# Performance work log

Hardware: AMD Instinct MI355X
Metric: run time of the kernel (lower is better)

## Reference

```python
import jax, jax.numpy as jnp
import numpy as np

NUM_HEADS = 12


def setup_inputs() -> dict:
    key = jax.random.key(0)
    ks = jax.random.split(key, 6)
    B, N, C, CNN = 64, 576, 768, 2048
    return {
        "image_patches": jax.random.normal(ks[0], (B, N, C), dtype=jnp.float32),
        "cnn_feature_vector": jax.random.normal(ks[1], (B, CNN), dtype=jnp.float32),
        "Wq": jax.random.normal(ks[2], (C, C), dtype=jnp.float32) * (C ** -0.5),
        "Wkv": jax.random.normal(ks[3], (CNN, 2 * C), dtype=jnp.float32) * (CNN ** -0.5),
        "Wp": jax.random.normal(ks[4], (C, C), dtype=jnp.float32) * (C ** -0.5),
        "bp": jnp.zeros((C,), dtype=jnp.float32),
    }


def reference(image_patches, cnn_feature_vector, Wq, Wkv, Wp, bp):
    B, N, C = image_patches.shape
    H = NUM_HEADS
    D = C // H
    scale = D ** -0.5
    # Q projection: [B, N, C] -> [B, N, H, D]
    q = (image_patches @ Wq).reshape(B, N, H, D)
    # KV projection from single CNN feature (KV seq len == 1): [B, 2C]
    kv = cnn_feature_vector @ Wkv
    k = kv[:, :C].reshape(B, H, D)  # [B, H, D]
    v = kv[:, C:].reshape(B, H, D)  # [B, H, D]
    # attn logits: q . k over head_dim -> [B, N, H, 1]; softmax over kv_len=1
    logits = jnp.einsum("bnhd,bhd->bnh", q, k)[..., None] * scale
    attn = jax.nn.softmax(logits, axis=-1)  # degenerate: all ones
    # attn @ v with kv_len 1 -> broadcast v over N
    x = (attn * v[:, None, :, :]).reshape(B, N, C)
    # output projection (dropout is identity in eval)
    return x @ Wp + bp
```

## Files before the change

kernel.cpp:

```cpp
#include <hip/hip_runtime.h>


#define B_DIM   64
#define N_DIM   576
#define C_DIM   768
#define CNN_DIM 2048
#define C4_DIM  192

typedef float f4 __attribute__((ext_vector_type(4)));

__global__ __launch_bounds__(256) void proj_v_kernel(
    const float* __restrict__ cnn, const float* __restrict__ Wkv,
    float* __restrict__ v)
{
    __shared__ f4 red[32 * 64];

    int tid = threadIdx.x;
    int c4l = tid & 7;
    int s   = tid >> 3;
    int bg  = blockIdx.x & 7;
    int cg  = blockIdx.x >> 3;
    int b0  = bg * 8;
    int c4  = cg * 8 + c4l;
    int k0  = s * 64;

    const f4* w4 = (const f4*)(Wkv + C_DIM);

    f4 acc[8];
#pragma unroll
    for (int i = 0; i < 8; ++i) acc[i] = (f4)0.f;

#pragma unroll 4
    for (int kk = 0; kk < 64; ++kk) {
        int k = k0 + kk;
        f4 w = w4[k * 384 + c4];
#pragma unroll
        for (int i = 0; i < 8; ++i) {
            float a = cnn[(b0 + i) * CNN_DIM + k];
            acc[i] += a * w;
        }
    }

#pragma unroll
    for (int i = 0; i < 8; ++i) red[s * 64 + i * 8 + c4l] = acc[i];
    __syncthreads();

#pragma unroll
    for (int step = 16; step >= 1; step >>= 1) {
        if (s < step) {
#pragma unroll
            for (int i = 0; i < 8; ++i)
                red[s * 64 + i * 8 + c4l] += red[(s + step) * 64 + i * 8 + c4l];
        }
        __syncthreads();
    }

    if (tid < 64) {
        int i  = tid >> 3;
        int cl = tid & 7;
        *(f4*)(v + (b0 + i) * C_DIM + (cg * 8 + cl) * 4) = red[i * 8 + cl];
    }
}

__global__ __launch_bounds__(256) void proj_y_kernel(
    const float* __restrict__ v, const float* __restrict__ Wp,
    const float* __restrict__ bp, float* __restrict__ y)
{
    __shared__ f4 red[32 * 64];

    int tid = threadIdx.x;
    int c4l = tid & 7;
    int s   = tid >> 3;
    int bg  = blockIdx.x & 7;
    int cg  = blockIdx.x >> 3;
    int b0  = bg * 8;
    int c4  = cg * 8 + c4l;
    int k0  = s * 24;

    const f4* w4 = (const f4*)Wp;

    f4 acc[8];
#pragma unroll
    for (int i = 0; i < 8; ++i) acc[i] = (f4)0.f;

#pragma unroll 4
    for (int kk = 0; kk < 24; ++kk) {
        int k = k0 + kk;
        f4 w = w4[k * C4_DIM + c4];
#pragma unroll
        for (int i = 0; i < 8; ++i) {
            float a = v[(b0 + i) * C_DIM + k];
            acc[i] += a * w;
        }
    }

#pragma unroll
    for (int i = 0; i < 8; ++i) red[s * 64 + i * 8 + c4l] = acc[i];
    __syncthreads();

#pragma unroll
    for (int step = 16; step >= 1; step >>= 1) {
        if (s < step) {
#pragma unroll
            for (int i = 0; i < 8; ++i)
                red[s * 64 + i * 8 + c4l] += red[(s + step) * 64 + i * 8 + c4l];
        }
        __syncthreads();
    }

    if (tid < 64) {
        int i  = tid >> 3;
        int cl = tid & 7;
        f4 r  = red[i * 8 + cl];
        f4 bb = *(const f4*)(bp + (cg * 8 + cl) * 4);
        r += bb;
        *(f4*)(y + (b0 + i) * C_DIM + (cg * 8 + cl) * 4) = r;
    }
}

__global__ __launch_bounds__(256) void bcast_kernel(
    const f4* __restrict__ y4, f4* __restrict__ out)
{
    int idx = blockIdx.x * 256 + threadIdx.x;
    int c4  = idx % C4_DIM;
    int b   = idx / (N_DIM * C4_DIM);
    f4 r = y4[b * C4_DIM + c4];
    __builtin_nontemporal_store(r, &out[idx]);
}

extern "C" void kernel_launch(void* const* d_in, const int* in_sizes, int n_in,
                              void* d_out, int out_size, void* d_ws, size_t ws_size,
                              hipStream_t stream)
{
    const float* cnn = (const float*)d_in[1];
    const float* Wkv = (const float*)d_in[3];
    const float* Wp  = (const float*)d_in[4];
    const float* bp  = (const float*)d_in[5];

    float* v = (float*)d_ws;
    float* y = v + B_DIM * C_DIM;

    proj_v_kernel<<<192, 256, 0, stream>>>(cnn, Wkv, v);
    proj_y_kernel<<<192, 256, 0, stream>>>(v, Wp, bp, y);

    int n_out4 = B_DIM * N_DIM * C4_DIM;
    bcast_kernel<<<n_out4 / 256, 256, 0, stream>>>((const f4*)y, (f4*)d_out);
}
```

Before: 232.5 us.

## Fuse output projection with broadcast store into one kernel

Merges the y = v@Wp + bp projection and the broadcast-to-N write into one kernel with a (12, 64) grid. Each block computes one batch's 64-column slice of y, reduces it in shared memory, then writes it across all 576 rows. This removes a kernel launch and the round trip of y through global memory. In exchange, each block re-reads a column slice of Wp for a single batch, so the GEMV loses batch reuse, and the store phase runs on only 768 blocks.

```diff
diff --git a/kernel.cpp b/kernel.cpp
--- a/kernel.cpp
+++ b/kernel.cpp
@@ -62,70 +62,48 @@
     }
 }
 
-__global__ __launch_bounds__(256) void proj_y_kernel(
+__global__ __launch_bounds__(256) void proj_bcast_kernel(
     const float* __restrict__ v, const float* __restrict__ Wp,
-    const float* __restrict__ bp, float* __restrict__ y)
+    const float* __restrict__ bp, f4* __restrict__ out)
 {
-    __shared__ f4 red[32 * 64];
+    __shared__ f4 red[16 * 16];
 
     int tid = threadIdx.x;
-    int c4l = tid & 7;
-    int s   = tid >> 3;
-    int bg  = blockIdx.x & 7;
-    int cg  = blockIdx.x >> 3;
-    int b0  = bg * 8;
-    int c4  = cg * 8 + c4l;
-    int k0  = s * 24;
+    int col = tid & 15;
+    int ks  = tid >> 4;
+    int ct  = blockIdx.x;
+    int b   = blockIdx.y;
 
-    const f4* w4 = (const f4*)Wp;
+    const f4* wp4 = (const f4*)Wp;
+    const float* vb = v + b * C_DIM;
 
-    f4 acc[8];
-#pragma unroll
-    for (int i = 0; i < 8; ++i) acc[i] = (f4)0.f;
-
+    f4 acc = (f4)0.f;
+    int wcol = ct * 16 + col;
 #pragma unroll 4
-    for (int kk = 0; kk < 24; ++kk) {
-        int k = k0 + kk;
-        f4 w = w4[k * C4_DIM + c4];
-#pragma unroll
-        for (int i = 0; i < 8; ++i) {
-            float a = v[(b0 + i) * C_DIM + k];
-            acc[i] += a * w;
-        }
+    for (int kk = 0; kk < 48; ++kk) {
+        int k = ks * 48 + kk;
+        acc += vb[k] * wp4[k * C4_DIM + wcol];
     }
-
-#pragma unroll
-    for (int i = 0; i < 8; ++i) red[s * 64 + i * 8 + c4l] = acc[i];
+    red[ks * 16 + col] = acc;
     __syncthreads();
 
 #pragma unroll
-    for (int step = 16; step >= 1; step >>= 1) {
-        if (s < step) {
-#pragma unroll
-            for (int i = 0; i < 8; ++i)
-                red[s * 64 + i * 8 + c4l] += red[(s + step) * 64 + i * 8 + c4l];
-        }
+    for (int step = 8; step >= 1; step >>= 1) {
+        if (ks < step)
+            red[ks * 16 + col] += red[(ks + step) * 16 + col];
         __syncthreads();
     }
+    if (tid < 16)
+        red[tid] += ((const f4*)bp)[ct * 16 + tid];
+    __syncthreads();
 
-    if (tid < 64) {
-        int i  = tid >> 3;
-        int cl = tid & 7;
-        f4 r  = red[i * 8 + cl];
-        f4 bb = *(const f4*)(bp + (cg * 8 + cl) * 4);
-        r += bb;
-        *(f4*)(y + (b0 + i) * C_DIM + (cg * 8 + cl) * 4) = r;
+    f4 yv = red[col];
+    f4* base = out + (size_t)b * (N_DIM * C4_DIM) + ct * 16 + col;
+    int nrow = tid >> 4;
+#pragma unroll 4
+    for (int iter = 0; iter < 36; ++iter) {
+        __builtin_nontemporal_store(yv, base + (nrow + iter * 16) * C4_DIM);
     }
-}
-
-__global__ __launch_bounds__(256) void bcast_kernel(
-    const f4* __restrict__ y4, f4* __restrict__ out)
-{
-    int idx = blockIdx.x * 256 + threadIdx.x;
-    int c4  = idx % C4_DIM;
-    int b   = idx / (N_DIM * C4_DIM);
-    f4 r = y4[b * C4_DIM + c4];
-    __builtin_nontemporal_store(r, &out[idx]);
 }
 
 extern "C" void kernel_launch(void* const* d_in, const int* in_sizes, int n_in,
@@ -138,11 +116,7 @@
     const float* bp  = (const float*)d_in[5];
 
     float* v = (float*)d_ws;
-    float* y = v + B_DIM * C_DIM;
 
     proj_v_kernel<<<192, 256, 0, stream>>>(cnn, Wkv, v);
-    proj_y_kernel<<<192, 256, 0, stream>>>(v, Wp, bp, y);
-
-    int n_out4 = B_DIM * N_DIM * C4_DIM;
-    bcast_kernel<<<n_out4 / 256, 256, 0, stream>>>((const f4*)y, (f4*)d_out);
+    proj_bcast_kernel<<<dim3(12, 64), 256, 0, stream>>>(v, Wp, bp, (f4*)d_out);
 }
```

New measurement: 229.9 us. Within noise of the previous version (-1.1%).
